# Kernel optimization log

Measured on AMD Instinct MI355X. Metric: run time of the kernel, lower is better.

## Reference

```python
import jax, jax.numpy as jnp
import numpy as np

D_MODEL = 1024
NUM_HEADS = 16
HEAD_DIM = D_MODEL // NUM_HEADS


def setup_inputs() -> dict:
    key = jax.random.key(0)
    k_x, k_wqkv, k_bqkv, k_wfc, k_bfc = jax.random.split(key, 5)
    scale_in = 1.0 / np.sqrt(D_MODEL)
    return {
        "x": jax.random.normal(k_x, (2, 2048, D_MODEL), dtype=jnp.float32),
        # torch nn.Linear stores weight as [out_features, in_features]
        "w_qkv": jax.random.uniform(k_wqkv, (3 * D_MODEL, D_MODEL), jnp.float32, -scale_in, scale_in),
        "b_qkv": jax.random.uniform(k_bqkv, (3 * D_MODEL,), jnp.float32, -scale_in, scale_in),
        "w_fc": jax.random.uniform(k_wfc, (D_MODEL, D_MODEL), jnp.float32, -scale_in, scale_in),
        "b_fc": jax.random.uniform(k_bfc, (D_MODEL,), jnp.float32, -scale_in, scale_in),
    }


def reference(x, w_qkv, b_qkv, w_fc, b_fc):
    B, S, _ = x.shape
    # fused QKV projection: [B,S,3*d_model]
    qkv = jnp.einsum("bsd,ed->bse", x, w_qkv) + b_qkv
    # [B,S,H,3*head_dim] -> [B,H,S,3*head_dim]
    qkv = qkv.reshape(B, S, NUM_HEADS, 3 * HEAD_DIM).transpose(0, 2, 1, 3)
    Q, K, V = jnp.split(qkv, 3, axis=-1)  # each [B,H,S,head_dim]
    scores = jnp.einsum("bhqd,bhkd->bhqk", Q, K) / np.sqrt(HEAD_DIM).astype(np.float32)
    attention = jax.nn.softmax(scores, axis=-1)  # [B,H,S,S]
    values = jnp.einsum("bhqk,bhkd->bhqd", attention, V)
    # [B,H,S,head_dim] -> [B,S,d_model]
    values = values.transpose(0, 2, 1, 3).reshape(B, S, D_MODEL)
    out = jnp.einsum("bsd,ed->bse", values, w_fc) + b_fc
    return out
```

## Files before the change

kernel.cpp:

```cpp
#include <hip/hip_runtime.h>
#include <hip/hip_bf16.h>
#include <hip/hip_fp16.h>

#define D_MODEL 1024
#define NH 16
#define HD 64
#define BATCH 2
#define SEQ 2048

typedef __attribute__((ext_vector_type(8))) short short8;
typedef __attribute__((ext_vector_type(4))) float floatx4;
typedef __attribute__((ext_vector_type(8))) _Float16 half8;

static __device__ __forceinline__ short f2bf(float f) {
    __hip_bfloat16 h = __float2bfloat16(f);
    return *reinterpret_cast<short*>(&h);
}
static __device__ __forceinline__ unsigned int pk2bf(float a, float b) {
    float2 t; t.x = a; t.y = b;
    __hip_bfloat162 h2 = __float22bfloat162_rn(t);
    return *reinterpret_cast<unsigned int*>(&h2);
}

#define GLDS(gp, lp) __builtin_amdgcn_global_load_lds( \
    (const __attribute__((address_space(1))) void*)(gp), \
    (__attribute__((address_space(3))) void*)(lp), 16, 0, 0)

__global__ __launch_bounds__(256) void cvt_all(
    const float* __restrict__ x, const float* __restrict__ wq,
    const float* __restrict__ wf,
    short* __restrict__ Xb, short* __restrict__ Wqb, short* __restrict__ Wfb)
{
    int i = blockIdx.x * 256 + threadIdx.x;
    const float* src; short* dst; int off;
    if (i < 524288)      { src = x;  dst = Xb;  off = i; }
    else if (i < 917504) { src = wq; dst = Wqb; off = i - 524288; }
    else                 { src = wf; dst = Wfb; off = i - 917504; }
    float4 a = *reinterpret_cast<const float4*>(src + off * 8);
    float4 b = *reinterpret_cast<const float4*>(src + off * 8 + 4);
    short8 o;
    o[0] = f2bf(a.x); o[1] = f2bf(a.y); o[2] = f2bf(a.z); o[3] = f2bf(a.w);
    o[4] = f2bf(b.x); o[5] = f2bf(b.y); o[6] = f2bf(b.z); o[7] = f2bf(b.w);
    *reinterpret_cast<short8*>(dst + off * 8) = o;
}

__global__ __launch_bounds__(256) void qkv_gemm(
    const short* __restrict__ X, const short* __restrict__ W,
    const float* __restrict__ bias,
    short* __restrict__ Qs, short* __restrict__ Ks, short* __restrict__ Vt_g)
{
    __shared__ __align__(16) short As[128][72];
    __shared__ __align__(16) short Bs[128 * 64];
    const int tid = threadIdx.x;
    const int m0 = blockIdx.y * 128;
    const int n0 = blockIdx.x * 128;
    const int bi = m0 >> 11, sl0 = m0 & 2047;
    const int w = tid >> 6, lane = tid & 63;
    const int quad = lane >> 4, l15 = lane & 15;
    const int wm2 = w >> 1, wn2 = w & 1;
    short* Asl = &As[0][0];

    const int rg = lane >> 3;
    const int sl = lane & 7;
    const int cg = sl ^ rg;

    floatx4 acc[4][4];
#pragma unroll
    for (int i = 0; i < 4; i++)
#pragma unroll
        for (int j = 0; j < 4; j++) acc[i][j] = (floatx4)0.0f;

    for (int k0 = 0; k0 < 1024; k0 += 64) {
        __syncthreads();
#pragma unroll
        for (int j = 0; j < 4; j++) {
            int g = w * 4 + j;
            int r = g * 8 + rg;
            GLDS(&X[(size_t)(m0 + r) * 1024 + k0 + cg * 8], &Asl[g * 512]);
            GLDS(&W[(size_t)(n0 + r) * 1024 + k0 + cg * 8], &Bs[g * 512]);
        }
        __syncthreads();
#pragma unroll
        for (int kk = 0; kk < 2; kk++) {
            short8 a[4], b[4];
#pragma unroll
            for (int t = 0; t < 4; t++) {
                int swz = ((kk * 4 + quad) ^ (l15 & 7)) * 8;
                a[t] = *reinterpret_cast<const short8*>(
                    &Asl[(wm2 * 64 + t * 16 + l15) * 64 + swz]);
                b[t] = *reinterpret_cast<const short8*>(
                    &Bs[(wn2 * 64 + t * 16 + l15) * 64 + swz]);
            }
#pragma unroll
            for (int mt = 0; mt < 4; mt++)
#pragma unroll
                for (int nt = 0; nt < 4; nt++)
                    acc[mt][nt] = __builtin_amdgcn_mfma_f32_16x16x32_bf16(
                        a[mt], b[nt], acc[mt][nt], 0, 0, 0);
        }
    }

    __syncthreads();
    short* T = &As[0][0];
#pragma unroll
    for (int half = 0; half < 2; half++) {
        const int colg0 = n0 + half * 64;
        const int h = colg0 / 192;
        const int t = (colg0 % 192) / 64;
        if (wn2 == half) {
#pragma unroll
            for (int nt = 0; nt < 4; nt++) {
                int jj = nt * 16 + l15;
                float bv = bias[colg0 + jj];
#pragma unroll
                for (int mt = 0; mt < 4; mt++) {
#pragma unroll
                    for (int r = 0; r < 4; r++) {
                        int ml = wm2 * 64 + mt * 16 + quad * 4 + r;
                        float v = acc[mt][nt][r] + bv;
                        if (t == 0) v *= 0.18033688f;
                        if (t < 2) As[ml][jj] = f2bf(v);
                        else       T[jj * 136 + ml] = f2bf(v);
                    }
                }
            }
        }
        __syncthreads();
        if (t < 2) {
            short* dst = (t == 0) ? Qs : Ks;
#pragma unroll
            for (int i = 0; i < 4; i++) {
                int c = tid + i * 256;
                int row = c >> 3, ck = c & 7;
                uint4 u = *reinterpret_cast<const uint4*>(&As[row][ck * 8]);
                *reinterpret_cast<uint4*>(
                    &dst[((size_t)(bi * NH + h) * SEQ + sl0 + row) * HD + ck * 8]) = u;
            }
        } else {
#pragma unroll
            for (int i = 0; i < 4; i++) {
                int c = tid + i * 256;
                int d = c >> 4, ck = c & 15;
                uint4 u = *reinterpret_cast<const uint4*>(&T[d * 136 + ck * 8]);
                *reinterpret_cast<uint4*>(
                    &Vt_g[((size_t)(bi * NH + h) * HD + d) * SEQ + sl0 + ck * 8]) = u;
            }
        }
        __syncthreads();
    }
}

__global__ __launch_bounds__(256, 4) void attn_kernel(
    const short* __restrict__ Qs, const short* __restrict__ Ks,
    const short* __restrict__ Vt_g,
    _Float16* __restrict__ Opart, float* __restrict__ lpart)
{
    __shared__ __align__(16) short Kl[64][72];
    __shared__ __align__(16) short Vt[64][72];
    __shared__ __align__(16) short Pl[4][32][72];

    const int tid = threadIdx.x;
    const int w = tid >> 6, lane = tid & 63;
    const int quad = lane >> 4, l15 = lane & 15;
    const int bx = blockIdx.x;
    const int khalf = bx & 1;
    const int q0 = (bx >> 1) * 128;
    const int h = blockIdx.y, bi = blockIdx.z;
    const int bh = bi * NH + h;
    const int kbase = bh * SEQ * HD;
    const int vbase = bh * HD * SEQ;
    const int kt0 = khalf * (SEQ / 2);

    const int kr0 = tid >> 3,         kc0 = (tid & 7) * 8;
    const int kr1 = (tid + 256) >> 3, kc1 = (tid & 7) * 8;

    const short8 onesv = {(short)0x3F80, (short)0x3F80, (short)0x3F80, (short)0x3F80,
                          (short)0x3F80, (short)0x3F80, (short)0x3F80, (short)0x3F80};

    short8 aq[2][2];
#pragma unroll
    for (int qt2 = 0; qt2 < 2; qt2++) {
        const short* qp = Qs + kbase + (q0 + w * 32 + qt2 * 16 + l15) * HD;
#pragma unroll
        for (int c = 0; c < 2; c++)
            aq[qt2][c] = *reinterpret_cast<const short8*>(qp + c * 32 + quad * 8);
    }

    floatx4 o[2][4], ol[2];
#pragma unroll
    for (int mt = 0; mt < 2; mt++) {
        ol[mt] = (floatx4)0.0f;
#pragma unroll
        for (int nt = 0; nt < 4; nt++) o[mt][nt] = (floatx4)0.0f;
    }

    for (int it = 0; it < SEQ / 128; it++) {
        const int kt = kt0 + it * 64;
        __syncthreads();
        *reinterpret_cast<uint4*>(&Kl[kr0][kc0]) =
            *reinterpret_cast<const uint4*>(&Ks[kbase + (kt + kr0) * HD + kc0]);
        *reinterpret_cast<uint4*>(&Kl[kr1][kc1]) =
            *reinterpret_cast<const uint4*>(&Ks[kbase + (kt + kr1) * HD + kc1]);
        *reinterpret_cast<uint4*>(&Vt[kr0][kc0]) =
            *reinterpret_cast<const uint4*>(&Vt_g[vbase + kr0 * SEQ + kt + kc0]);
        *reinterpret_cast<uint4*>(&Vt[kr1][kc1]) =
            *reinterpret_cast<const uint4*>(&Vt_g[vbase + kr1 * SEQ + kt + kc1]);
        __syncthreads();

        floatx4 sf[4][2];
#pragma unroll
        for (int kt2 = 0; kt2 < 4; kt2++)
#pragma unroll
            for (int qt2 = 0; qt2 < 2; qt2++) sf[kt2][qt2] = (floatx4)0.0f;
#pragma unroll
        for (int c = 0; c < 2; c++) {
#pragma unroll
            for (int kt2 = 0; kt2 < 4; kt2++) {
                short8 bk = *reinterpret_cast<const short8*>(
                    &Kl[kt2 * 16 + l15][c * 32 + quad * 8]);
#pragma unroll
                for (int qt2 = 0; qt2 < 2; qt2++)
                    sf[kt2][qt2] = __builtin_amdgcn_mfma_f32_16x16x32_bf16(
                        bk, aq[qt2][c], sf[kt2][qt2], 0, 0, 0);
            }
        }

#pragma unroll
        for (int kt2 = 0; kt2 < 4; kt2++) {
#pragma unroll
            for (int qt2 = 0; qt2 < 2; qt2++) {
                uint2 p;
                p.x = pk2bf(exp2f(sf[kt2][qt2][0]), exp2f(sf[kt2][qt2][1]));
                p.y = pk2bf(exp2f(sf[kt2][qt2][2]), exp2f(sf[kt2][qt2][3]));
                *reinterpret_cast<uint2*>(&Pl[w][qt2 * 16 + l15][kt2 * 16 + quad * 4]) = p;
            }
        }
        asm volatile("s_waitcnt lgkmcnt(0)" ::: "memory");

#pragma unroll
        for (int c = 0; c < 2; c++) {
            short8 vf[4];
#pragma unroll
            for (int nt = 0; nt < 4; nt++)
                vf[nt] = *reinterpret_cast<const short8*>(
                    &Vt[nt * 16 + l15][c * 32 + quad * 8]);
#pragma unroll
            for (int mt = 0; mt < 2; mt++) {
                short8 ap = *reinterpret_cast<const short8*>(
                    &Pl[w][mt * 16 + l15][c * 32 + quad * 8]);
#pragma unroll
                for (int nt = 0; nt < 4; nt++)
                    o[mt][nt] = __builtin_amdgcn_mfma_f32_16x16x32_bf16(
                        ap, vf[nt], o[mt][nt], 0, 0, 0);
                ol[mt] = __builtin_amdgcn_mfma_f32_16x16x32_bf16(
                    ap, onesv, ol[mt], 0, 0, 0);
            }
        }
    }

#pragma unroll
    for (int mt = 0; mt < 2; mt++) {
#pragma unroll
        for (int r = 0; r < 4; r++) {
            int ql = q0 + w * 32 + mt * 16 + quad * 4 + r;
            size_t base = (size_t)khalf * (4096u * 1024u) +
                          ((size_t)bi * SEQ + ql) * D_MODEL + h * HD;
#pragma unroll
            for (int nt = 0; nt < 4; nt++)
                Opart[base + nt * 16 + l15] = (_Float16)o[mt][nt][r];
            if (l15 == 0)
                lpart[khalf * 65536 + bh * SEQ + ql] = ol[mt][r];
        }
    }
}

__global__ __launch_bounds__(256) void combine_kernel(
    const _Float16* __restrict__ O, const float* __restrict__ lp,
    short* __restrict__ attnb)
{
    int i = blockIdx.x * 256 + threadIdx.x;
    int m = i >> 7;
    int e0 = (i & 127) * 8;
    int bi = m >> 11, s = m & 2047, h = e0 >> 6;
    int bh = bi * NH + h;
    float l = lp[bh * SEQ + s] + lp[65536 + bh * SEQ + s];
    float rl = 1.0f / l;
    size_t off = (size_t)m * D_MODEL + e0;
    half8 a = *reinterpret_cast<const half8*>(O + off);
    half8 b = *reinterpret_cast<const half8*>(O + 4096u * 1024u + off);
    short8 out;
#pragma unroll
    for (int j = 0; j < 8; j++)
        out[j] = f2bf(((float)a[j] + (float)b[j]) * rl);
    *reinterpret_cast<short8*>(attnb + off) = out;
}

__global__ __launch_bounds__(256) void fc_gemm(
    const short* __restrict__ A, const short* __restrict__ W,
    const float* __restrict__ bias, float* __restrict__ out)
{
    __shared__ __align__(16) short As[128 * 64];
    __shared__ __align__(16) short Bs[64 * 64];
    const int tid = threadIdx.x;
    const int m0 = blockIdx.y * 128;
    const int n0 = blockIdx.x * 64;
    const int w = tid >> 6, lane = tid & 63;
    const int quad = lane >> 4, l15 = lane & 15;
    const int wm2 = w >> 1, wn2 = w & 1;

    const int rg = lane >> 3;
    const int sl = lane & 7;
    const int cg = sl ^ rg;

    floatx4 acc[4][2];
#pragma unroll
    for (int i = 0; i < 4; i++)
#pragma unroll
        for (int j = 0; j < 2; j++) acc[i][j] = (floatx4)0.0f;

    for (int k0 = 0; k0 < 1024; k0 += 64) {
        __syncthreads();
#pragma unroll
        for (int j = 0; j < 4; j++) {
            int g = w * 4 + j;
            int r = g * 8 + rg;
            GLDS(&A[(size_t)(m0 + r) * 1024 + k0 + cg * 8], &As[g * 512]);
        }
#pragma unroll
        for (int j = 0; j < 2; j++) {
            int g = w * 2 + j;
            int r = g * 8 + rg;
            GLDS(&W[(size_t)(n0 + r) * 1024 + k0 + cg * 8], &Bs[g * 512]);
        }
        __syncthreads();
#pragma unroll
        for (int kk = 0; kk < 2; kk++) {
            int swz = ((kk * 4 + quad) ^ (l15 & 7)) * 8;
            short8 a[4], b[2];
#pragma unroll
            for (int i = 0; i < 4; i++)
                a[i] = *reinterpret_cast<const short8*>(
                    &As[(wm2 * 64 + i * 16 + l15) * 64 + swz]);
#pragma unroll
            for (int j = 0; j < 2; j++)
                b[j] = *reinterpret_cast<const short8*>(
                    &Bs[(wn2 * 32 + j * 16 + l15) * 64 + swz]);
#pragma unroll
            for (int mt = 0; mt < 4; mt++)
#pragma unroll
                for (int nt = 0; nt < 2; nt++)
                    acc[mt][nt] = __builtin_amdgcn_mfma_f32_16x16x32_bf16(
                        a[mt], b[nt], acc[mt][nt], 0, 0, 0);
        }
    }

#pragma unroll
    for (int nt = 0; nt < 2; nt++) {
        int col = n0 + wn2 * 32 + nt * 16 + l15;
        float bv = bias[col];
#pragma unroll
        for (int mt = 0; mt < 4; mt++) {
#pragma unroll
            for (int r = 0; r < 4; r++) {
                int row = m0 + wm2 * 64 + mt * 16 + quad * 4 + r;
                out[row * 1024 + col] = acc[mt][nt][r] + bv;
            }
        }
    }
}

extern "C" void kernel_launch(void* const* d_in, const int* in_sizes, int n_in,
                              void* d_out, int out_size, void* d_ws, size_t ws_size,
                              hipStream_t stream) {
    const float* x     = (const float*)d_in[0];
    const float* w_qkv = (const float*)d_in[1];
    const float* b_qkv = (const float*)d_in[2];
    const float* w_fc  = (const float*)d_in[3];
    const float* b_fc  = (const float*)d_in[4];
    float* out = (float*)d_out;

    const size_t M1 = 1024u * 1024u;
    short* ws = (short*)d_ws;
    short* Qs    = ws;
    short* Ks    = ws + 4 * M1;
    short* Vt_g  = ws + 8 * M1;
    short* Wfb   = ws + 12 * M1;
    short* Xb    = ws + 13 * M1;
    short* Wqb   = ws + 17 * M1;
    _Float16* Opart = (_Float16*)(ws + 13 * M1);
    float* lpart = (float*)(ws + 21 * M1);
    short* attnb = Qs;

    cvt_all<<<4096, 256, 0, stream>>>(x, w_qkv, w_fc, Xb, Wqb, Wfb);
    qkv_gemm<<<dim3(24, 32), 256, 0, stream>>>(Xb, Wqb, b_qkv, Qs, Ks, Vt_g);
    attn_kernel<<<dim3(32, 16, 2), 256, 0, stream>>>(Qs, Ks, Vt_g, Opart, lpart);
    combine_kernel<<<2048, 256, 0, stream>>>(Opart, lpart, attnb);
    fc_gemm<<<dim3(16, 32), 256, 0, stream>>>(attnb, Wfb, b_fc, out);
}
```

Before: 217.4 us.

## Double attention query tile per block to reuse K/V tiles across more rows

Each attention block now handles 256 queries (64 per wave) instead of 128, halving the grid and the number of times each K/V tile is loaded from global memory into shared memory. K fragments are hoisted into registers once per tile and reused across four query subtiles, and the P buffer is enlarged to match. The trade-off is higher register and LDS use per block (launch bound lowered to 2 blocks/SM) and only 512 blocks, which reduces occupancy and latency hiding.

```diff
diff --git a/kernel.cpp b/kernel.cpp
--- a/kernel.cpp
+++ b/kernel.cpp
@@ -150,21 +150,21 @@
     }
 }
 
-__global__ __launch_bounds__(256, 4) void attn_kernel(
+__global__ __launch_bounds__(256, 2) void attn_kernel(
     const short* __restrict__ Qs, const short* __restrict__ Ks,
     const short* __restrict__ Vt_g,
     _Float16* __restrict__ Opart, float* __restrict__ lpart)
 {
     __shared__ __align__(16) short Kl[64][72];
     __shared__ __align__(16) short Vt[64][72];
-    __shared__ __align__(16) short Pl[4][32][72];
+    __shared__ __align__(16) short Pl[4][64][72];
 
     const int tid = threadIdx.x;
     const int w = tid >> 6, lane = tid & 63;
     const int quad = lane >> 4, l15 = lane & 15;
     const int bx = blockIdx.x;
     const int khalf = bx & 1;
-    const int q0 = (bx >> 1) * 128;
+    const int q0 = (bx >> 1) * 256;
     const int h = blockIdx.y, bi = blockIdx.z;
     const int bh = bi * NH + h;
     const int kbase = bh * SEQ * HD;
@@ -177,21 +177,21 @@
     const short8 onesv = {(short)0x3F80, (short)0x3F80, (short)0x3F80, (short)0x3F80,
                           (short)0x3F80, (short)0x3F80, (short)0x3F80, (short)0x3F80};
 
-    short8 aq[2][2];
-#pragma unroll
-    for (int qt2 = 0; qt2 < 2; qt2++) {
-        const short* qp = Qs + kbase + (q0 + w * 32 + qt2 * 16 + l15) * HD;
+    short8 aq[4][2];
+#pragma unroll
+    for (int qt2 = 0; qt2 < 4; qt2++) {
+        const short* qp = Qs + kbase + (q0 + w * 64 + qt2 * 16 + l15) * HD;
 #pragma unroll
         for (int c = 0; c < 2; c++)
             aq[qt2][c] = *reinterpret_cast<const short8*>(qp + c * 32 + quad * 8);
     }
 
-    floatx4 o[2][4], ol[2];
-#pragma unroll
-    for (int mt = 0; mt < 2; mt++) {
-        ol[mt] = (floatx4)0.0f;
-#pragma unroll
-        for (int nt = 0; nt < 4; nt++) o[mt][nt] = (floatx4)0.0f;
+    floatx4 o[4][4], ol[4];
+#pragma unroll
+    for (int qt2 = 0; qt2 < 4; qt2++) {
+        ol[qt2] = (floatx4)0.0f;
+#pragma unroll
+        for (int nt = 0; nt < 4; nt++) o[qt2][nt] = (floatx4)0.0f;
     }
 
     for (int it = 0; it < SEQ / 128; it++) {
@@ -207,32 +207,32 @@
             *reinterpret_cast<const uint4*>(&Vt_g[vbase + kr1 * SEQ + kt + kc1]);
         __syncthreads();
 
-        floatx4 sf[4][2];
+        short8 bk[4][2];
 #pragma unroll
         for (int kt2 = 0; kt2 < 4; kt2++)
 #pragma unroll
-            for (int qt2 = 0; qt2 < 2; qt2++) sf[kt2][qt2] = (floatx4)0.0f;
-#pragma unroll
-        for (int c = 0; c < 2; c++) {
+            for (int c = 0; c < 2; c++)
+                bk[kt2][c] = *reinterpret_cast<const short8*>(
+                    &Kl[kt2 * 16 + l15][c * 32 + quad * 8]);
+
+#pragma unroll
+        for (int qt2 = 0; qt2 < 4; qt2++) {
+            floatx4 sf[4];
+#pragma unroll
+            for (int kt2 = 0; kt2 < 4; kt2++) sf[kt2] = (floatx4)0.0f;
+#pragma unroll
+            for (int c = 0; c < 2; c++)
+#pragma unroll
+                for (int kt2 = 0; kt2 < 4; kt2++)
+                    sf[kt2] = __builtin_amdgcn_mfma_f32_16x16x32_bf16(
+                        bk[kt2][c], aq[qt2][c], sf[kt2], 0, 0, 0);
 #pragma unroll
             for (int kt2 = 0; kt2 < 4; kt2++) {
-                short8 bk = *reinterpret_cast<const short8*>(
-                    &Kl[kt2 * 16 + l15][c * 32 + quad * 8]);
-#pragma unroll
-                for (int qt2 = 0; qt2 < 2; qt2++)
-                    sf[kt2][qt2] = __builtin_amdgcn_mfma_f32_16x16x32_bf16(
-                        bk, aq[qt2][c], sf[kt2][qt2], 0, 0, 0);
-            }
-        }
-
-#pragma unroll
-        for (int kt2 = 0; kt2 < 4; kt2++) {
-#pragma unroll
-            for (int qt2 = 0; qt2 < 2; qt2++) {
                 uint2 p;
-                p.x = pk2bf(exp2f(sf[kt2][qt2][0]), exp2f(sf[kt2][qt2][1]));
-                p.y = pk2bf(exp2f(sf[kt2][qt2][2]), exp2f(sf[kt2][qt2][3]));
-                *reinterpret_cast<uint2*>(&Pl[w][qt2 * 16 + l15][kt2 * 16 + quad * 4]) = p;
+                p.x = pk2bf(exp2f(sf[kt2][0]), exp2f(sf[kt2][1]));
+                p.y = pk2bf(exp2f(sf[kt2][2]), exp2f(sf[kt2][3]));
+                *reinterpret_cast<uint2*>(
+                    &Pl[w][qt2 * 16 + l15][kt2 * 16 + quad * 4]) = p;
             }
         }
         asm volatile("s_waitcnt lgkmcnt(0)" ::: "memory");
@@ -245,31 +245,31 @@
                 vf[nt] = *reinterpret_cast<const short8*>(
                     &Vt[nt * 16 + l15][c * 32 + quad * 8]);
 #pragma unroll
-            for (int mt = 0; mt < 2; mt++) {
+            for (int qt2 = 0; qt2 < 4; qt2++) {
                 short8 ap = *reinterpret_cast<const short8*>(
-                    &Pl[w][mt * 16 + l15][c * 32 + quad * 8]);
+                    &Pl[w][qt2 * 16 + l15][c * 32 + quad * 8]);
 #pragma unroll
                 for (int nt = 0; nt < 4; nt++)
-                    o[mt][nt] = __builtin_amdgcn_mfma_f32_16x16x32_bf16(
-                        ap, vf[nt], o[mt][nt], 0, 0, 0);
-                ol[mt] = __builtin_amdgcn_mfma_f32_16x16x32_bf16(
-                    ap, onesv, ol[mt], 0, 0, 0);
-            }
-        }
-    }
-
-#pragma unroll
-    for (int mt = 0; mt < 2; mt++) {
+                    o[qt2][nt] = __builtin_amdgcn_mfma_f32_16x16x32_bf16(
+                        ap, vf[nt], o[qt2][nt], 0, 0, 0);
+                ol[qt2] = __builtin_amdgcn_mfma_f32_16x16x32_bf16(
+                    ap, onesv, ol[qt2], 0, 0, 0);
+            }
+        }
+    }
+
+#pragma unroll
+    for (int qt2 = 0; qt2 < 4; qt2++) {
 #pragma unroll
         for (int r = 0; r < 4; r++) {
-            int ql = q0 + w * 32 + mt * 16 + quad * 4 + r;
+            int ql = q0 + w * 64 + qt2 * 16 + quad * 4 + r;
             size_t base = (size_t)khalf * (4096u * 1024u) +
                           ((size_t)bi * SEQ + ql) * D_MODEL + h * HD;
 #pragma unroll
             for (int nt = 0; nt < 4; nt++)
-                Opart[base + nt * 16 + l15] = (_Float16)o[mt][nt][r];
+                Opart[base + nt * 16 + l15] = (_Float16)o[qt2][nt][r];
             if (l15 == 0)
-                lpart[khalf * 65536 + bh * SEQ + ql] = ol[mt][r];
+                lpart[khalf * 65536 + bh * SEQ + ql] = ol[qt2][r];
         }
     }
 }
@@ -393,7 +393,7 @@
 
     cvt_all<<<4096, 256, 0, stream>>>(x, w_qkv, w_fc, Xb, Wqb, Wfb);
     qkv_gemm<<<dim3(24, 32), 256, 0, stream>>>(Xb, Wqb, b_qkv, Qs, Ks, Vt_g);
-    attn_kernel<<<dim3(32, 16, 2), 256, 0, stream>>>(Qs, Ks, Vt_g, Opart, lpart);
+    attn_kernel<<<dim3(16, 16, 2), 256, 0, stream>>>(Qs, Ks, Vt_g, Opart, lpart);
     combine_kernel<<<2048, 256, 0, stream>>>(Opart, lpart, attnb);
     fc_gemm<<<dim3(16, 32), 256, 0, stream>>>(attnb, Wfb, b_fc, out);
 }
```

Measured after the change: 215.4 us. About the same (-0.9%).
